# Kernel optimization log

Hardware: AMD Instinct MI355X
Metric: run time of the kernel (lower is better)

## Reference

```python
import jax, jax.numpy as jnp
import numpy as np
from jax import lax

NUM_HEADS = 6
LN_EPS = 1e-5


def _ln(x, g, b):
    mu = jnp.mean(x, axis=-1, keepdims=True)
    var = jnp.mean(jnp.square(x - mu), axis=-1, keepdims=True)
    return (x - mu) * jax.lax.rsqrt(var + LN_EPS) * g + b


def _gelu(x):
    return jax.nn.gelu(x, approximate=False)


def setup_inputs() -> dict:
    key = jax.random.key(0)
    ks = jax.random.split(key, 16)
    B, N, C = 16, 1025, 384
    hid = 4 * C  # 1536
    k3 = 3  # depthwise kernel size
    s = 0.02
    rn = lambda k, shape: (jax.random.normal(k, shape, jnp.float32) * s)
    return {
        "x": jax.random.normal(ks[0], (B, N, C), jnp.float32),
        "ln1_g": jnp.ones((C,), jnp.float32),
        "ln1_b": jnp.zeros((C,), jnp.float32),
        "qkv_w": rn(ks[1], (3 * C, C)),
        "proj_w": rn(ks[2], (C, C)),
        "proj_b": jnp.zeros((C,), jnp.float32),
        "ln2_g": jnp.ones((C,), jnp.float32),
        "ln2_b": jnp.zeros((C,), jnp.float32),
        "conv1_w": rn(ks[3], (hid, C)),          # 1x1 conv as matrix
        "conv1_b": jnp.zeros((hid,), jnp.float32),
        "conv2_w": rn(ks[4], (hid, 1, k3, k3)),   # depthwise OIHW
        "conv2_b": jnp.zeros((hid,), jnp.float32),
        "conv3_w": rn(ks[5], (C, hid)),           # 1x1 conv as matrix
        "conv3_b": jnp.zeros((C,), jnp.float32),
        "bn1_s": jnp.ones((hid,), jnp.float32), "bn1_b": jnp.zeros((hid,), jnp.float32),
        "bn2_s": jnp.ones((hid,), jnp.float32), "bn2_b": jnp.zeros((hid,), jnp.float32),
        "bn3_s": jnp.ones((C,), jnp.float32), "bn3_b": jnp.zeros((C,), jnp.float32),
        "comp_w": rn(ks[6], (C // 4, C)), "comp_b": jnp.zeros((C // 4,), jnp.float32),
        "exc_w": rn(ks[7], (C, C // 4)), "exc_b": jnp.zeros((C,), jnp.float32),
    }


def _block(x, ln1_g, ln1_b, qkv_w, proj_w, proj_b, ln2_g, ln2_b,
           conv1_w, conv1_b, conv2_w, conv2_b, conv3_w, conv3_b,
           bn1_s, bn1_b, bn2_s, bn2_b, bn3_s, bn3_b,
           comp_w, comp_b, exc_w, exc_b):
    B, N, C = x.shape
    Hh = NUM_HEADS
    hd = C // Hh
    S = int(np.sqrt(N - 1))

    # ---- Attention (manual softmax(QK^T)V) ----
    h = _ln(x, ln1_g, ln1_b)
    qkv = jnp.einsum('bnc,dc->bnd', h, qkv_w).reshape(B, N, 3, Hh, hd)
    qkv = qkv.transpose(2, 0, 3, 1, 4)  # [3,B,H,N,hd]
    q, k, v = qkv[0], qkv[1], qkv[2]
    attn = jax.nn.softmax(jnp.einsum('bhqd,bhkd->bhqk', q, k) * (hd ** -0.5), axis=-1)
    o = jnp.einsum('bhqk,bhkd->bhqd', attn, v).transpose(0, 2, 1, 3).reshape(B, N, C)
    o = o @ proj_w.T + proj_b
    x = x + o

    # ---- DAFF FFN (conv + BN(eval affine) + GELU + SE gating on cls) ----
    h2 = _ln(x, ln2_g, ln2_b)
    cls_tok, tok = h2[:, :1], h2[:, 1:]
    t = tok.reshape(B, S, S, C).transpose(0, 3, 1, 2)  # NCHW
    hid = conv1_w.shape[0]
    y = jnp.einsum('bchw,oc->bohw', t, conv1_w) + conv1_b[None, :, None, None]
    y = y * bn1_s[None, :, None, None] + bn1_b[None, :, None, None]
    y = _gelu(y)
    shortcut = y
    y = lax.conv_general_dilated(y, conv2_w, (1, 1), 'SAME',
                                 feature_group_count=hid,
                                 dimension_numbers=('NCHW', 'OIHW', 'NCHW'))
    y = y + conv2_b[None, :, None, None]
    y = y * bn2_s[None, :, None, None] + bn2_b[None, :, None, None]
    y = shortcut + _gelu(y)
    y = jnp.einsum('bchw,oc->bohw', y, conv3_w) + conv3_b[None, :, None, None]
    y = y * bn3_s[None, :, None, None] + bn3_b[None, :, None, None]
    # SE gate on cls token
    w = jnp.mean(y, axis=(2, 3)).reshape(B, 1, C)
    w = _gelu(w @ comp_w.T + comp_b) @ exc_w.T + exc_b
    cls_out = cls_tok * w
    tok_out = y.reshape(B, C, S * S).transpose(0, 2, 1)
    out = jnp.concatenate([cls_out, tok_out], axis=1)
    return x + out


def reference(x, ln1_g, ln1_b, qkv_w, proj_w, proj_b, ln2_g, ln2_b,
              conv1_w, conv1_b, conv2_w, conv2_b, conv3_w, conv3_b,
              bn1_s, bn1_b, bn2_s, bn2_b, bn3_s, bn3_b,
              comp_w, comp_b, exc_w, exc_b):
    return _block(x, ln1_g, ln1_b, qkv_w, proj_w, proj_b, ln2_g, ln2_b,
                  conv1_w, conv1_b, conv2_w, conv2_b, conv3_w, conv3_b,
                  bn1_s, bn1_b, bn2_s, bn2_b, bn3_s, bn3_b,
                  comp_w, comp_b, exc_w, exc_b)
```

## Files before the change

### kernel.cpp

```cpp
#include <hip/hip_runtime.h>
#include <math.h>

#define DI __device__ __forceinline__

namespace {

constexpr int B_ = 16;
constexpr int N_ = 1025;
constexpr int C_ = 384;
constexpr int H_ = 6;
constexpr int HD_ = 64;
constexpr int HID_ = 1536;
constexpr int P_ = 1024;
constexpr int MTOK = B_ * P_;
constexpr int MALL = B_ * N_;
constexpr int NPAD = 1088;
constexpr long long AF = (long long)MALL * C_;

constexpr int NQKV = 3 * C_ * C_;
constexpr int NPROJ = C_ * C_;
constexpr int NC1 = HID_ * C_;
constexpr int NC3 = C_ * HID_;
constexpr int NW2 = HID_ * 9;
constexpr int T1 = NQKV, T2 = T1 + NPROJ, T3 = T2 + NC1, T4 = T3 + NC3;
constexpr int T5 = T4 + NW2, T6 = T5 + HID_;

typedef __attribute__((ext_vector_type(4))) float f32x4;
typedef __attribute__((ext_vector_type(8))) short bf16x8;

DI float gelu_f(float x) { return 0.5f * x * (1.0f + erff(x * 0.7071067811865475f)); }

DI float us2f(unsigned short u) {
  union { unsigned int i; float f; } c; c.i = ((unsigned)u) << 16; return c.f;
}
DI unsigned short f2us(float f) {
  union { float f; unsigned int i; } c; c.f = f;
  unsigned int r = c.i + 0x7FFF + ((c.i >> 16) & 1);
  return (unsigned short)(r >> 16);
}
DI unsigned short f2us_trunc(float f) {
  union { float f; unsigned int i; } c; c.f = f;
  return (unsigned short)(c.i >> 16);
}
DI void bf8_to_f(const uint4 v, float* f) {
  const unsigned int u[4] = {v.x, v.y, v.z, v.w};
#pragma unroll
  for (int t = 0; t < 4; t++) {
    union { unsigned int i; float fl; } lo, hi;
    lo.i = (u[t] & 0xffffu) << 16;
    hi.i = u[t] & 0xffff0000u;
    f[2 * t] = lo.fl; f[2 * t + 1] = hi.fl;
  }
}
DI uint4 f_to_bf8(const float* f) {
  unsigned int w[4];
#pragma unroll
  for (int t = 0; t < 4; t++)
    w[t] = (unsigned)f2us(f[2 * t]) | ((unsigned)f2us(f[2 * t + 1]) << 16);
  return make_uint4(w[0], w[1], w[2], w[3]);
}

DI void gl2lds16(const unsigned short* g, unsigned short* l) {
  __builtin_amdgcn_global_load_lds(
      (const __attribute__((address_space(1))) void*)g,
      (__attribute__((address_space(3))) void*)l, 16, 0, 0);
}

__global__ __launch_bounds__(256) void cvtall_kernel(
    const float* __restrict__ qkv_w, const float* __restrict__ proj_w,
    const float* __restrict__ conv1_w, const float* __restrict__ conv3_w,
    const float* __restrict__ conv2_w, const float* __restrict__ c2b,
    const float* __restrict__ s2, const float* __restrict__ b2,
    unsigned short* __restrict__ dst16, float* __restrict__ Bc)
{
  const int idx = blockIdx.x * 256 + threadIdx.x;
  if (idx < T1)      dst16[idx] = f2us(qkv_w[idx]);
  else if (idx < T2) dst16[idx] = f2us(proj_w[idx - T1]);
  else if (idx < T3) dst16[idx] = f2us(conv1_w[idx - T2]);
  else if (idx < T4) dst16[idx] = f2us(conv3_w[idx - T3]);
  else if (idx < T5) {
    const int r = idx - T4, tap = r / HID_, c = r % HID_;
    dst16[idx] = f2us(conv2_w[c * 9 + tap] * s2[c]);
  } else if (idx < T6) {
    const int c = idx - T5;
    Bc[c] = c2b[c] * s2[c] + b2[c];
  }
}

__global__ __launch_bounds__(256) void lnw_kernel(
    const float* __restrict__ x, const float* __restrict__ g,
    const float* __restrict__ b, unsigned short* __restrict__ out,
    float* __restrict__ cls_out, int nrows)
{
  const int row = blockIdx.x * 4 + (threadIdx.x >> 6);
  if (row >= nrows) return;
  const int lane = threadIdx.x & 63;
  const float* xr = x + (long long)row * C_;
  float v[6];
#pragma unroll
  for (int i = 0; i < 6; i++) v[i] = xr[lane + 64 * i];
  float s = 0.f, q = 0.f;
#pragma unroll
  for (int i = 0; i < 6; i++) { s += v[i]; q += v[i] * v[i]; }
#pragma unroll
  for (int m = 1; m < 64; m <<= 1) {
    s += __shfl_xor(s, m, 64);
    q += __shfl_xor(q, m, 64);
  }
  const float mean = s * (1.0f / C_);
  const float var  = q * (1.0f / C_) - mean * mean;
  const float rstd = rsqrtf(var + 1e-5f);
  unsigned short* orow = out + (long long)row * C_;
  const bool iscls = (cls_out != nullptr) && (row % N_) == 0;
  float* cr = iscls ? cls_out + (long long)(row / N_) * C_ : nullptr;
#pragma unroll
  for (int i = 0; i < 6; i++) {
    const int c = lane + 64 * i;
    const float r = (v[i] - mean) * rstd * g[c] + b[c];
    orow[c] = f2us(r);
    if (iscls) cr[c] = r;
  }
}

__global__ __launch_bounds__(256) void vtrans_kernel(
    const unsigned short* __restrict__ v, unsigned short* __restrict__ vt)
{
  __shared__ unsigned short t[64][72];
  const int bh = blockIdx.x, nt = blockIdx.y;
  const int n0 = nt * 64;
  const int tid = threadIdx.x;
  {
    const int nl = tid >> 2;
    const int dc = (tid & 3) * 16;
    const int gn = n0 + nl;
    uint4 a = make_uint4(0u,0u,0u,0u), b = make_uint4(0u,0u,0u,0u);
    if (gn < N_) {
      const unsigned short* p = v + ((long long)bh * N_ + gn) * HD_ + dc;
      a = *(const uint4*)p; b = *(const uint4*)(p + 8);
    }
    *(uint4*)&t[nl][dc] = a;
    *(uint4*)&t[nl][dc + 8] = b;
  }
  __syncthreads();
  {
    const int dl = tid >> 2;
    const int nc = (tid & 3) * 16;
    unsigned short tmp[16];
#pragma unroll
    for (int i = 0; i < 16; i++) tmp[i] = t[nc + i][dl];
    unsigned short* p = vt + ((long long)bh * HD_ + dl) * NPAD + n0 + nc;
    *(uint4*)p = *(uint4*)&tmp[0];
    *(uint4*)(p + 8) = *(uint4*)&tmp[8];
  }
}

enum { GM_QKV = 0, GM_PROJ = 1, GM_CONV1 = 2, GM_CONV3 = 3 };

template <int MODE, int K>
__global__ __launch_bounds__(256) void mgemm_kernel(
    const unsigned short* __restrict__ A, const unsigned short* __restrict__ W,
    void* __restrict__ o0, void* __restrict__ o1, void* __restrict__ o2,
    const float* __restrict__ e0, const float* __restrict__ e1,
    const float* __restrict__ e2, int M)
{
  __shared__ unsigned short As[128][64];
  __shared__ unsigned short Bs[128][64];
  const int m0 = blockIdx.x * 128, n0 = blockIdx.y * 128;
  if (m0 >= M) return;
  const int tid = threadIdx.x;
  const int lane = tid & 63, wv = tid >> 6;
  const int lane15 = lane & 15, quad = lane >> 4;
  const int wm = (wv >> 1) * 64, wn = (wv & 1) * 64;

  const unsigned short* agp[4];
  const unsigned short* bgp[4];
#pragma unroll
  for (int t = 0; t < 4; t++) {
    const int lr = wv * 32 + t * 8 + (lane >> 3);
    const int chunk = (lane & 7) ^ (lr & 7);
    int gm = m0 + lr;
    if (gm > M - 1) gm = M - 1;
    long long arow = gm;
    if constexpr (MODE == GM_CONV1) arow = (long long)(gm >> 10) * N_ + 1 + (gm & 1023);
    agp[t] = A + arow * K + chunk * 8;
    bgp[t] = W + (long long)(n0 + lr) * K + chunk * 8;
  }

  f32x4 acc[4][4];
#pragma unroll
  for (int i = 0; i < 4; i++)
#pragma unroll
    for (int j = 0; j < 4; j++) acc[i][j] = (f32x4)0.f;

  const int xsel = lane15 & 7;
  for (int k0 = 0; k0 < K; k0 += 64) {
    __syncthreads();
#pragma unroll
    for (int t = 0; t < 4; t++) {
      gl2lds16(agp[t] + k0, &As[wv * 32 + t * 8][0]);
      gl2lds16(bgp[t] + k0, &Bs[wv * 32 + t * 8][0]);
    }
    __syncthreads();
#pragma unroll
    for (int kh = 0; kh < 2; kh++) {
      bf16x8 af[4], bfr[4];
#pragma unroll
      for (int i = 0; i < 4; i++)
        af[i] = *(const bf16x8*)&As[wm + i * 16 + lane15][((kh * 4 + quad) ^ xsel) * 8];
#pragma unroll
      for (int j = 0; j < 4; j++)
        bfr[j] = *(const bf16x8*)&Bs[wn + j * 16 + lane15][((kh * 4 + quad) ^ xsel) * 8];
#pragma unroll
      for (int i = 0; i < 4; i++)
#pragma unroll
        for (int j = 0; j < 4; j++)
          acc[i][j] = __builtin_amdgcn_mfma_f32_16x16x32_bf16(af[i], bfr[j], acc[i][j], 0, 0, 0);
    }
  }
#pragma unroll
  for (int i = 0; i < 4; i++) {
#pragma unroll
    for (int r = 0; r < 4; r++) {
      const int m = m0 + wm + i * 16 + quad * 4 + r;
      if (m >= M) continue;
#pragma unroll
      for (int j = 0; j < 4; j++) {
        const int n = n0 + wn + j * 16 + lane15;
        const float val = acc[i][j][r];
        if constexpr (MODE == GM_QKV) {
          const int which = n / C_, rr = n % C_, hh = rr >> 6, e = rr & 63;
          const int b = m / N_, nn = m % N_;
          unsigned short* dst = (unsigned short*)((which == 0) ? o0 : ((which == 1) ? o1 : o2));
          const float sval = (which == 0) ? val * 0.18033688f : val;
          dst[(((long long)b * H_ + hh) * N_ + nn) * HD_ + e] = f2us(sval);
        } else if constexpr (MODE == GM_PROJ) {
          ((float*)o0)[(long long)m * C_ + n] = val + e0[(long long)m * C_ + n] + e1[n];
        } else if constexpr (MODE == GM_CONV1) {
          ((unsigned short*)o0)[(long long)m * HID_ + n] =
              f2us(gelu_f((val + e0[n]) * e1[n] + e2[n]));
        } else {
          const float val2 = (val + e0[n]) * e1[n] + e2[n];
          ((float*)o0)[(long long)m * C_ + n] = val2;
          const int bb = m >> 10, pp = m & 1023;
          const long long orow = ((long long)bb * N_ + 1 + pp) * C_ + n;
          ((float*)o1)[orow] = ((const float*)o2)[orow] + val2;
        }
      }
    }
  }
}

__global__ __launch_bounds__(512) void fattn_kernel(
    const unsigned short* __restrict__ q, const unsigned short* __restrict__ k,
    const unsigned short* __restrict__ vt, unsigned short* __restrict__ o)
{
  __shared__ unsigned short Ks[2][64][64];
  __shared__ unsigned short Vt[2][64][64];
  __shared__ unsigned short Ps[8][16][72];
  const int tid = threadIdx.x;
  const int lane = tid & 63, wv = tid >> 6;
  const int lane15 = lane & 15, quad = lane >> 4;
  const int bh = blockIdx.x, qt = blockIdx.y;
  const long long headoff = (long long)bh * N_;
  const int q0 = qt * 128 + wv * 16;

  int gq0 = q0 + lane15;
  if (gq0 > N_ - 1) gq0 = N_ - 1;
  const long long qrow = headoff + gq0;
  const bf16x8 aq0 = *(const bf16x8*)(q + qrow * HD_ + quad * 8);
  const bf16x8 aq1 = *(const bf16x8*)(q + qrow * HD_ + 32 + quad * 8);

  const int srow = wv * 8 + (lane >> 3);
  const int ch = (lane & 7) ^ (srow & 7);
  const unsigned short* kgp = k + (headoff + srow) * HD_ + ch * 8;
  const unsigned short* vgp = vt + ((long long)bh * HD_ + srow) * NPAD + ch * 8;

  f32x4 O[4];
  float l_r[4] = {0.f, 0.f, 0.f, 0.f};
#pragma unroll
  for (int n = 0; n < 4; n++) O[n] = (f32x4)0.f;

  const int xsel = lane15 & 7;

  gl2lds16(kgp, &Ks[0][wv * 8][0]);
  gl2lds16(vgp, &Vt[0][wv * 8][0]);
  __syncthreads();

  for (int kt = 0; kt < 17; kt++) {
    const int cur = kt & 1;
    if (kt < 16) {
      const long long koff = (long long)(kt + 1) * 64;
      gl2lds16(kgp + koff * HD_, &Ks[cur ^ 1][wv * 8][0]);
      gl2lds16(vgp + koff, &Vt[cur ^ 1][wv * 8][0]);
    }

    f32x4 S[4];
    __builtin_amdgcn_s_setprio(1);
#pragma unroll
    for (int n = 0; n < 4; n++) {
      S[n] = (f32x4)0.f;
      const bf16x8 b0 = *(const bf16x8*)&Ks[cur][n * 16 + lane15][(quad ^ xsel) * 8];
      S[n] = __builtin_amdgcn_mfma_f32_16x16x32_bf16(aq0, b0, S[n], 0, 0, 0);
      const bf16x8 b1 = *(const bf16x8*)&Ks[cur][n * 16 + lane15][((4 + quad) ^ xsel) * 8];
      S[n] = __builtin_amdgcn_mfma_f32_16x16x32_bf16(aq1, b1, S[n], 0, 0, 0);
    }
    __builtin_amdgcn_s_setprio(0);
    if (kt == 16) {
#pragma unroll
      for (int n = 0; n < 4; n++) {
        if ((kt * 64 + n * 16 + lane15) >= N_)
#pragma unroll
          for (int r = 0; r < 4; r++) S[n][r] = -1e30f;
      }
    }
#pragma unroll
    for (int n = 0; n < 4; n++)
#pragma unroll
      for (int r = 0; r < 4; r++) {
        const float p = exp2f(S[n][r]);
        l_r[r] += p;
        Ps[wv][quad * 4 + r][n * 16 + lane15] = f2us_trunc(p);
      }
    __builtin_amdgcn_s_setprio(1);
#pragma unroll
    for (int half = 0; half < 2; half++) {
      const bf16x8 ap = *(const bf16x8*)&Ps[wv][lane15][half * 32 + quad * 8];
#pragma unroll
      for (int n = 0; n < 4; n++) {
        const bf16x8 bv =
            *(const bf16x8*)&Vt[cur][n * 16 + lane15][(((half * 4 + quad)) ^ xsel) * 8];
        O[n] = __builtin_amdgcn_mfma_f32_16x16x32_bf16(ap, bv, O[n], 0, 0, 0);
      }
    }
    __builtin_amdgcn_s_setprio(0);
    __syncthreads();
  }
#pragma unroll
  for (int msk = 1; msk < 16; msk <<= 1)
#pragma unroll
    for (int r = 0; r < 4; r++) l_r[r] += __shfl_xor(l_r[r], msk, 64);

  const int b = bh / H_, hh = bh % H_;
#pragma unroll
  for (int r = 0; r < 4; r++) {
    const int gq = q0 + quad * 4 + r;
    if (gq < N_) {
      const float inv = 1.0f / l_r[r];
#pragma unroll
      for (int n = 0; n < 4; n++)
        o[((long long)b * N_ + gq) * C_ + hh * HD_ + n * 16 + lane15] = f2us(O[n][r] * inv);
    }
  }
}

__global__ __launch_bounds__(192) void dwconv_kernel(
    const unsigned short* __restrict__ y1, const unsigned short* __restrict__ w2s,
    const float* __restrict__ Bc, unsigned short* __restrict__ y2)
{
  const int jp = blockIdx.x & 15;
  const int i  = (blockIdx.x >> 4) & 31;
  const int b  = blockIdx.x >> 9;
  const int j0 = jp * 2;
  const int cb = threadIdx.x << 3;

  float wf[9][8];
#pragma unroll
  for (int tap = 0; tap < 9; tap++) {
    const uint4 wv = *(const uint4*)(w2s + tap * HID_ + cb);
    bf8_to_f(wv, wf[tap]);
  }
  float acc0[8] = {}, acc1[8] = {};
  float sh0[8], sh1[8];
#pragma unroll
  for (int di = -1; di <= 1; di++) {
    const int ii = i + di;
    if (ii < 0 || ii > 31) continue;
    const long long rowbase = ((long long)b * P_ + ii * 32) * HID_ + cb;
#pragma unroll
    for (int dj = -1; dj <= 2; dj++) {
      const int jj = j0 + dj;
      if (jj < 0 || jj > 31) continue;
      const uint4 dv = *(const uint4*)(y1 + rowbase + (long long)jj * HID_);
      float df[8]; bf8_to_f(dv, df);
      if (dj <= 1) {
        const int tap = (di + 1) * 3 + (dj + 1);
#pragma unroll
        for (int t = 0; t < 8; t++) acc0[t] += df[t] * wf[tap][t];
      }
      if (dj >= 0) {
        const int tap = (di + 1) * 3 + dj;
#pragma unroll
        for (int t = 0; t < 8; t++) acc1[t] += df[t] * wf[tap][t];
      }
      if (di == 0 && dj == 0) {
#pragma unroll
        for (int t = 0; t < 8; t++) sh0[t] = df[t];
      }
      if (di == 0 && dj == 1) {
#pragma unroll
        for (int t = 0; t < 8; t++) sh1[t] = df[t];
      }
    }
  }
  const float4 bc0 = *(const float4*)(Bc + cb);
  const float4 bc1 = *(const float4*)(Bc + cb + 4);
  const float bcv[8] = {bc0.x, bc0.y, bc0.z, bc0.w, bc1.x, bc1.y, bc1.z, bc1.w};
  float of0[8], of1[8];
#pragma unroll
  for (int t = 0; t < 8; t++) {
    of0[t] = sh0[t] + gelu_f(acc0[t] + bcv[t]);
    of1[t] = sh1[t] + gelu_f(acc1[t] + bcv[t]);
  }
  const long long tok0 = ((long long)b * P_ + i * 32 + j0) * HID_ + cb;
  *(uint4*)(y2 + tok0) = f_to_bf8(of0);
  *(uint4*)(y2 + tok0 + HID_) = f_to_bf8(of1);
}

__global__ __launch_bounds__(384) void pool_kernel(const float* __restrict__ y3,
                                                   float* __restrict__ w0p)
{
  const int b = blockIdx.x, chunk = blockIdx.y;
  const int c = threadIdx.x;
  float s = 0.f;
  for (int p = chunk * 64; p < chunk * 64 + 64; p++)
    s += y3[((long long)b * P_ + p) * C_ + c];
  w0p[((long long)b * 16 + chunk) * C_ + c] = s;
}

__global__ __launch_bounds__(128) void se_kernel(
    const float* __restrict__ w0p, const float* __restrict__ cw,
    const float* __restrict__ cb, const float* __restrict__ ew,
    const float* __restrict__ eb, float* __restrict__ wfin)
{
  __shared__ float wm[384];
  __shared__ float t1[96];
  const int b = blockIdx.x, t = threadIdx.x;
  for (int c = t; c < 384; c += 128) {
    float s = 0.f;
    for (int ch = 0; ch < 16; ch++) s += w0p[((long long)b * 16 + ch) * C_ + c];
    wm[c] = s * (1.0f / 1024.0f);
  }
  __syncthreads();
  if (t < 96) {
    float s = cb[t];
    for (int c = 0; c < 384; c++) s += wm[c] * cw[t * 384 + c];
    t1[t] = gelu_f(s);
  }
  __syncthreads();
  for (int c = t; c < 384; c += 128) {
    float s = eb[c];
    for (int j = 0; j < 96; j++) s += t1[j] * ew[c * 96 + j];
    wfin[(long long)b * C_ + c] = s;
  }
}

__global__ __launch_bounds__(256) void clsfix_kernel(
    const float* __restrict__ x2, const float* __restrict__ cls,
    const float* __restrict__ wfin, float* __restrict__ out)
{
  const int idx = blockIdx.x * 256 + threadIdx.x;
  if (idx >= B_ * C_) return;
  const int b = idx / C_, c = idx % C_;
  const long long row = (long long)b * N_ * C_ + c;
  out[row] = x2[row] + cls[idx] * wfin[idx];
}

}

extern "C" void kernel_launch(void* const* d_in, const int* in_sizes, int n_in,
                              void* d_out, int out_size, void* d_ws, size_t ws_size,
                              hipStream_t stream)
{
  const float* x       = (const float*)d_in[0];
  const float* ln1_g   = (const float*)d_in[1];
  const float* ln1_b   = (const float*)d_in[2];
  const float* qkv_w   = (const float*)d_in[3];
  const float* proj_w  = (const float*)d_in[4];
  const float* proj_b  = (const float*)d_in[5];
  const float* ln2_g   = (const float*)d_in[6];
  const float* ln2_b   = (const float*)d_in[7];
  const float* conv1_w = (const float*)d_in[8];
  const float* conv1_b = (const float*)d_in[9];
  const float* conv2_w = (const float*)d_in[10];
  const float* conv2_b = (const float*)d_in[11];
  const float* conv3_w = (const float*)d_in[12];
  const float* conv3_b = (const float*)d_in[13];
  const float* bn1_s   = (const float*)d_in[14];
  const float* bn1_b   = (const float*)d_in[15];
  const float* bn2_s   = (const float*)d_in[16];
  const float* bn2_b   = (const float*)d_in[17];
  const float* bn3_s   = (const float*)d_in[18];
  const float* bn3_b   = (const float*)d_in[19];
  const float* comp_w  = (const float*)d_in[20];
  const float* comp_b  = (const float*)d_in[21];
  const float* exc_w   = (const float*)d_in[22];
  const float* exc_b   = (const float*)d_in[23];

  char* wsb = (char*)d_ws;
  const size_t RA = 50331648, RB = 50331648, RC = 25190400;
  const size_t tailbytes = (size_t)T5 * 2 +
                           (size_t)(HID_ + B_ * C_ + B_ * 16 * C_ + B_ * C_) * 4;
  const size_t needed = RA + RB + RC + tailbytes;
  if (ws_size < needed) return;

  unsigned short* qb  = (unsigned short*)wsb;
  unsigned short* kb  = qb + AF;
  unsigned short* vb  = kb + AF;
  unsigned short* h2b = (unsigned short*)wsb;
  unsigned short* y2  = (unsigned short*)wsb;
  char* rb = wsb + RA;
  unsigned short* hb  = (unsigned short*)rb;
  unsigned short* o16 = (unsigned short*)rb;
  unsigned short* y1  = (unsigned short*)rb;
  float* y3           = (float*)rb;
  unsigned short* vtb = (unsigned short*)(wsb + RA + RB);
  float* x2 = (float*)(wsb + RA + RB);
  unsigned short* w16 = (unsigned short*)(wsb + RA + RB + RC);
  unsigned short* wqkv16  = w16;
  unsigned short* wproj16 = w16 + T1;
  unsigned short* wc116   = w16 + T2;
  unsigned short* wc316   = w16 + T3;
  unsigned short* w2s     = w16 + T4;
  float* Bc   = (float*)(w16 + T5);
  float* cls  = Bc + HID_;
  float* w0p  = cls + B_ * C_;
  float* wfin = w0p + B_ * 16 * C_;

  cvtall_kernel<<<(T6 + 255) / 256, 256, 0, stream>>>(
      qkv_w, proj_w, conv1_w, conv3_w, conv2_w, conv2_b, bn2_s, bn2_b, w16, Bc);
  lnw_kernel<<<(MALL + 3) / 4, 256, 0, stream>>>(x, ln1_g, ln1_b, hb, nullptr, MALL);
  mgemm_kernel<GM_QKV, 384><<<dim3(136, 9), 256, 0, stream>>>(
      hb, wqkv16, qb, kb, vb, nullptr, nullptr, nullptr, MALL);
  vtrans_kernel<<<dim3(B_ * H_, 17), 256, 0, stream>>>(vb, vtb);
  fattn_kernel<<<dim3(B_ * H_, 9), 512, 0, stream>>>(qb, kb, vtb, o16);
  mgemm_kernel<GM_PROJ, 384><<<dim3(136, 3), 256, 0, stream>>>(
      o16, wproj16, x2, nullptr, nullptr, x, proj_b, nullptr, MALL);
  lnw_kernel<<<(MALL + 3) / 4, 256, 0, stream>>>(x2, ln2_g, ln2_b, h2b, cls, MALL);
  mgemm_kernel<GM_CONV1, 384><<<dim3(128, 12), 256, 0, stream>>>(
      h2b, wc116, y1, nullptr, nullptr, conv1_b, bn1_s, bn1_b, MTOK);
  dwconv_kernel<<<B_ * 32 * 16, 192, 0, stream>>>(y1, w2s, Bc, y2);
  mgemm_kernel<GM_CONV3, 1536><<<dim3(128, 3), 256, 0, stream>>>(
      y2, wc316, y3, (float*)d_out, x2, conv3_b, bn3_s, bn3_b, MTOK);
  pool_kernel<<<dim3(B_, 16), 384, 0, stream>>>(y3, w0p);
  se_kernel<<<B_, 128, 0, stream>>>(w0p, comp_w, comp_b, exc_w, exc_b, wfin);
  clsfix_kernel<<<(B_ * C_ + 255) / 256, 256, 0, stream>>>(x2, cls, wfin, (float*)d_out);
}
```

Baseline: 414.9 us.

## Rewrite attention with 32x32 MFMA and register-resident P via permlane swap

The flash-attention kernel moves from 16x16x32 to 32x32x16 bf16 MFMA. It computes S transposed (K as the A operand) so the exponentiated P tile stays in registers, repacked with v_cvt_pk_bf16 and v_permlane32_swap, instead of a round trip through LDS. Blocks shrink to 4 waves of 32 queries each, and the per-row sum is rebroadcast with ds_bpermute. This removes the P shared-memory traffic and cuts MFMA issue count, but it uses more registers per wave, and in the last query tile some waves sit idle.

Measured after the change: 417.7 us. About the same (+0.7%).

```diff
diff --git a/kernel.cpp b/kernel.cpp
--- a/kernel.cpp
+++ b/kernel.cpp
@@ -26,6 +26,7 @@
 constexpr int T5 = T4 + NW2, T6 = T5 + HID_;
 
 typedef __attribute__((ext_vector_type(4))) float f32x4;
+typedef __attribute__((ext_vector_type(16))) float f32x16;
 typedef __attribute__((ext_vector_type(8))) short bf16x8;
 
 DI float gelu_f(float x) { return 0.5f * x * (1.0f + erff(x * 0.7071067811865475f)); }
@@ -58,6 +59,15 @@
   for (int t = 0; t < 4; t++)
     w[t] = (unsigned)f2us(f[2 * t]) | ((unsigned)f2us(f[2 * t + 1]) << 16);
   return make_uint4(w[0], w[1], w[2], w[3]);
+}
+
+DI unsigned cvt_pk_bf16(float lo, float hi) {
+  unsigned d;
+  asm("v_cvt_pk_bf16_f32 %0, %1, %2" : "=v"(d) : "v"(lo), "v"(hi));
+  return d;
+}
+DI void permswap(unsigned &a, unsigned &b) {
+  asm("v_permlane32_swap_b32 %0, %1" : "+v"(a), "+v"(b));
 }
 
 DI void gl2lds16(const unsigned short* g, unsigned short* l) {
@@ -250,105 +260,136 @@
   }
 }
 
-__global__ __launch_bounds__(512) void fattn_kernel(
+__global__ __launch_bounds__(256) void fattn_kernel(
     const unsigned short* __restrict__ q, const unsigned short* __restrict__ k,
     const unsigned short* __restrict__ vt, unsigned short* __restrict__ o)
 {
   __shared__ unsigned short Ks[2][64][64];
   __shared__ unsigned short Vt[2][64][64];
-  __shared__ unsigned short Ps[8][16][72];
   const int tid = threadIdx.x;
   const int lane = tid & 63, wv = tid >> 6;
-  const int lane15 = lane & 15, quad = lane >> 4;
+  const int lane31 = lane & 31, half = lane >> 5;
+  const int x7 = lane & 7;
   const int bh = blockIdx.x, qt = blockIdx.y;
   const long long headoff = (long long)bh * N_;
-  const int q0 = qt * 128 + wv * 16;
-
-  int gq0 = q0 + lane15;
-  if (gq0 > N_ - 1) gq0 = N_ - 1;
-  const long long qrow = headoff + gq0;
-  const bf16x8 aq0 = *(const bf16x8*)(q + qrow * HD_ + quad * 8);
-  const bf16x8 aq1 = *(const bf16x8*)(q + qrow * HD_ + 32 + quad * 8);
-
-  const int srow = wv * 8 + (lane >> 3);
-  const int ch = (lane & 7) ^ (srow & 7);
-  const unsigned short* kgp = k + (headoff + srow) * HD_ + ch * 8;
-  const unsigned short* vgp = vt + ((long long)bh * HD_ + srow) * NPAD + ch * 8;
-
-  f32x4 O[4];
-  float l_r[4] = {0.f, 0.f, 0.f, 0.f};
-#pragma unroll
-  for (int n = 0; n < 4; n++) O[n] = (f32x4)0.f;
-
-  const int xsel = lane15 & 7;
-
-  gl2lds16(kgp, &Ks[0][wv * 8][0]);
-  gl2lds16(vgp, &Vt[0][wv * 8][0]);
+  const int q0w = qt * 128 + wv * 32;
+  const bool active = q0w < N_;
+
+  int gq = q0w + lane31; if (gq > N_ - 1) gq = N_ - 1;
+  const unsigned short* qp = q + (headoff + gq) * HD_ + half * 8;
+  bf16x8 qf[4];
+#pragma unroll
+  for (int m = 0; m < 4; m++) qf[m] = *(const bf16x8*)(qp + m * 16);
+
+  const unsigned short* kgp[2];
+  const unsigned short* vgp[2];
+#pragma unroll
+  for (int t = 0; t < 2; t++) {
+    const int r = t * 32 + wv * 8 + (lane >> 3);
+    const int ch = (lane & 7) ^ (r & 7);
+    kgp[t] = k + (headoff + r) * HD_ + ch * 8;
+    vgp[t] = vt + ((long long)bh * HD_ + r) * NPAD + ch * 8;
+  }
+
+  f32x16 O0 = (f32x16)0.f, O1 = (f32x16)0.f;
+  float l = 0.f;
+
+#pragma unroll
+  for (int t = 0; t < 2; t++) {
+    gl2lds16(kgp[t], &Ks[0][t * 32 + wv * 8][0]);
+    gl2lds16(vgp[t], &Vt[0][t * 32 + wv * 8][0]);
+  }
   __syncthreads();
 
   for (int kt = 0; kt < 17; kt++) {
     const int cur = kt & 1;
     if (kt < 16) {
       const long long koff = (long long)(kt + 1) * 64;
-      gl2lds16(kgp + koff * HD_, &Ks[cur ^ 1][wv * 8][0]);
-      gl2lds16(vgp + koff, &Vt[cur ^ 1][wv * 8][0]);
-    }
-
-    f32x4 S[4];
-    __builtin_amdgcn_s_setprio(1);
-#pragma unroll
-    for (int n = 0; n < 4; n++) {
-      S[n] = (f32x4)0.f;
-      const bf16x8 b0 = *(const bf16x8*)&Ks[cur][n * 16 + lane15][(quad ^ xsel) * 8];
-      S[n] = __builtin_amdgcn_mfma_f32_16x16x32_bf16(aq0, b0, S[n], 0, 0, 0);
-      const bf16x8 b1 = *(const bf16x8*)&Ks[cur][n * 16 + lane15][((4 + quad) ^ xsel) * 8];
-      S[n] = __builtin_amdgcn_mfma_f32_16x16x32_bf16(aq1, b1, S[n], 0, 0, 0);
-    }
-    __builtin_amdgcn_s_setprio(0);
-    if (kt == 16) {
-#pragma unroll
-      for (int n = 0; n < 4; n++) {
-        if ((kt * 64 + n * 16 + lane15) >= N_)
-#pragma unroll
-          for (int r = 0; r < 4; r++) S[n][r] = -1e30f;
-      }
-    }
-#pragma unroll
-    for (int n = 0; n < 4; n++)
-#pragma unroll
-      for (int r = 0; r < 4; r++) {
-        const float p = exp2f(S[n][r]);
-        l_r[r] += p;
-        Ps[wv][quad * 4 + r][n * 16 + lane15] = f2us_trunc(p);
-      }
-    __builtin_amdgcn_s_setprio(1);
-#pragma unroll
-    for (int half = 0; half < 2; half++) {
-      const bf16x8 ap = *(const bf16x8*)&Ps[wv][lane15][half * 32 + quad * 8];
-#pragma unroll
-      for (int n = 0; n < 4; n++) {
-        const bf16x8 bv =
-            *(const bf16x8*)&Vt[cur][n * 16 + lane15][(((half * 4 + quad)) ^ xsel) * 8];
-        O[n] = __builtin_amdgcn_mfma_f32_16x16x32_bf16(ap, bv, O[n], 0, 0, 0);
-      }
-    }
-    __builtin_amdgcn_s_setprio(0);
+#pragma unroll
+      for (int t = 0; t < 2; t++) {
+        gl2lds16(kgp[t] + koff * HD_, &Ks[cur ^ 1][t * 32 + wv * 8][0]);
+        gl2lds16(vgp[t] + koff, &Vt[cur ^ 1][t * 32 + wv * 8][0]);
+      }
+    }
+    if (active) {
+      f32x16 S0 = (f32x16)0.f, S1 = (f32x16)0.f;
+      __builtin_amdgcn_s_setprio(1);
+#pragma unroll
+      for (int m = 0; m < 4; m++) {
+        const int chs = ((m * 2 + half) ^ x7) * 8;
+        const bf16x8 k0 = *(const bf16x8*)&Ks[cur][lane31][chs];
+        const bf16x8 k1 = *(const bf16x8*)&Ks[cur][32 + lane31][chs];
+        S0 = __builtin_amdgcn_mfma_f32_32x32x16_bf16(k0, qf[m], S0, 0, 0, 0);
+        S1 = __builtin_amdgcn_mfma_f32_32x32x16_bf16(k1, qf[m], S1, 0, 0, 0);
+      }
+      __builtin_amdgcn_s_setprio(0);
+      if (kt == 16) {
+#pragma unroll
+        for (int r = 0; r < 16; r++) {
+          const int kl = (r & 3) + 8 * (r >> 2) + 4 * half;
+          if (1024 + kl >= N_) S0[r] = -1e30f;
+          S1[r] = -1e30f;
+        }
+      }
+      unsigned pk0[8], pk1[8];
+#pragma unroll
+      for (int s = 0; s < 8; s++) {
+        const float a0 = exp2f(S0[2 * s]), a1 = exp2f(S0[2 * s + 1]);
+        const float b0 = exp2f(S1[2 * s]), b1 = exp2f(S1[2 * s + 1]);
+        l += (a0 + a1) + (b0 + b1);
+        pk0[s] = cvt_pk_bf16(a0, a1);
+        pk1[s] = cvt_pk_bf16(b0, b1);
+      }
+      unsigned wkc[4][4];
+#pragma unroll
+      for (int bb = 0; bb < 2; bb++) {
+#pragma unroll
+        for (int kc2 = 0; kc2 < 2; kc2++) {
+          unsigned a0 = bb ? pk1[kc2 * 4 + 0] : pk0[kc2 * 4 + 0];
+          unsigned a2 = bb ? pk1[kc2 * 4 + 2] : pk0[kc2 * 4 + 2];
+          permswap(a0, a2);
+          unsigned a1 = bb ? pk1[kc2 * 4 + 1] : pk0[kc2 * 4 + 1];
+          unsigned a3 = bb ? pk1[kc2 * 4 + 3] : pk0[kc2 * 4 + 3];
+          permswap(a1, a3);
+          const int kc = bb * 2 + kc2;
+          wkc[kc][0] = a0; wkc[kc][1] = a1; wkc[kc][2] = a2; wkc[kc][3] = a3;
+        }
+      }
+      __builtin_amdgcn_s_setprio(1);
+#pragma unroll
+      for (int kc = 0; kc < 4; kc++) {
+        union { unsigned u[4]; bf16x8 v; } pa;
+        pa.u[0] = wkc[kc][0]; pa.u[1] = wkc[kc][1];
+        pa.u[2] = wkc[kc][2]; pa.u[3] = wkc[kc][3];
+        const int chv = ((kc * 2 + half) ^ x7) * 8;
+        const bf16x8 v0 = *(const bf16x8*)&Vt[cur][lane31][chv];
+        const bf16x8 v1 = *(const bf16x8*)&Vt[cur][32 + lane31][chv];
+        O0 = __builtin_amdgcn_mfma_f32_32x32x16_bf16(pa.v, v0, O0, 0, 0, 0);
+        O1 = __builtin_amdgcn_mfma_f32_32x32x16_bf16(pa.v, v1, O1, 0, 0, 0);
+      }
+      __builtin_amdgcn_s_setprio(0);
+    }
     __syncthreads();
   }
-#pragma unroll
-  for (int msk = 1; msk < 16; msk <<= 1)
-#pragma unroll
-    for (int r = 0; r < 4; r++) l_r[r] += __shfl_xor(l_r[r], msk, 64);
-
+
+  l += __shfl_xor(l, 32, 64);
+  const float rinv = 1.0f / l;
+  float li[16];
+#pragma unroll
+  for (int r = 0; r < 16; r++) {
+    const int qloc = (r & 3) + 8 * (r >> 2) + 4 * half;
+    li[r] = __int_as_float(
+        __builtin_amdgcn_ds_bpermute(qloc * 4, __float_as_int(rinv)));
+  }
   const int b = bh / H_, hh = bh % H_;
 #pragma unroll
-  for (int r = 0; r < 4; r++) {
-    const int gq = q0 + quad * 4 + r;
-    if (gq < N_) {
-      const float inv = 1.0f / l_r[r];
-#pragma unroll
-      for (int n = 0; n < 4; n++)
-        o[((long long)b * N_ + gq) * C_ + hh * HD_ + n * 16 + lane15] = f2us(O[n][r] * inv);
+  for (int r = 0; r < 16; r++) {
+    const int qloc = (r & 3) + 8 * (r >> 2) + 4 * half;
+    const int gqr = q0w + qloc;
+    if (gqr < N_) {
+      const long long orow = ((long long)b * N_ + gqr) * C_ + hh * HD_;
+      o[orow + lane31] = f2us(O0[r] * li[r]);
+      o[orow + 32 + lane31] = f2us(O1[r] * li[r]);
     }
   }
 }
@@ -532,7 +573,7 @@
   mgemm_kernel<GM_QKV, 384><<<dim3(136, 9), 256, 0, stream>>>(
       hb, wqkv16, qb, kb, vb, nullptr, nullptr, nullptr, MALL);
   vtrans_kernel<<<dim3(B_ * H_, 17), 256, 0, stream>>>(vb, vtb);
-  fattn_kernel<<<dim3(B_ * H_, 9), 512, 0, stream>>>(qb, kb, vtb, o16);
+  fattn_kernel<<<dim3(B_ * H_, 9), 256, 0, stream>>>(qb, kb, vtb, o16);
   mgemm_kernel<GM_PROJ, 384><<<dim3(136, 3), 256, 0, stream>>>(
       o16, wproj16, x2, nullptr, nullptr, x, proj_b, nullptr, MALL);
   lnw_kernel<<<(MALL + 3) / 4, 256, 0, stream>>>(x2, ln2_g, ln2_b, h2b, cls, MALL);
```
